# Kernel optimization log

Measured on AMD Instinct MI355X. Metric: run time of the kernel, lower is better.

The kernel has to match this reference:

```python
import jax, jax.numpy as jnp
import numpy as np

N = 100000      # nodes
E = 1000000     # edges (nnz of adj)
DIN = 128
DOUT = 64
MAX_W = 0.05    # max_weight in project_column_stochastic


def setup_inputs() -> dict:
    key = jax.random.key(0)
    k1, k2, k3, k4 = jax.random.split(key, 4)
    x = jax.random.normal(k1, (N, DIN), dtype=jnp.float32)
    edge_index = jax.random.randint(k2, (2, E), 0, N)  # [2, E] (row, col) of sparse adj
    edge_vals = jax.random.uniform(k3, (E,), dtype=jnp.float32)
    # column-stochastic init, mirroring reset_parameters():
    # uniform(0,1) -> clamp(min=threshold=0, max=0.05) -> column normalize
    w = jax.random.uniform(k4, (DIN, DOUT), dtype=jnp.float32)
    w = jnp.clip(w, 0.0, MAX_W)
    w = w / jnp.clip(w.sum(axis=0, keepdims=True), 1e-8, None)
    bias = jnp.zeros((DOUT,), dtype=jnp.float32)
    return {"input": x, "edge_index": edge_index, "edge_vals": edge_vals,
            "weight": w, "bias": bias}


def reference(input, edge_index, edge_vals, weight, bias):
    # support = input @ weight  (dense projection)
    support = input @ weight                          # [N, DOUT]
    # output = spmm(adj, support): gather source rows, scale by nnz value,
    # scatter-add into destination rows.
    rows, cols = edge_index[0], edge_index[1]
    msgs = edge_vals[:, None] * support[cols]         # [E, DOUT]
    out = jax.ops.segment_sum(msgs, rows, num_segments=input.shape[0])  # [N, DOUT]
    return out + bias
```

## Files before the change

kernel.cpp:

```cpp
#include <hip/hip_runtime.h>
#include <hip/hip_bf16.h>

#define DIN 128
#define DOUT 64
#define BROWS 256
#define MAXBKT 512
#define NGEMM 391
#define PART_BLOCK 512
#define PART_VPT 8
#define PART_CHUNK (PART_BLOCK * PART_VPT)
#define CAP 3584
#define ACC_VPT 4
#define WSTRIDE 136

typedef short short8 __attribute__((ext_vector_type(8)));
typedef float f32x4 __attribute__((ext_vector_type(4)));

union U4S8 { uint4 u; short8 s; };
union BF2U { __hip_bfloat162 h; unsigned int u; };

__device__ inline unsigned int f2bf(float f) {
    union { float f; unsigned int u; } v; v.f = f;
    unsigned int u = v.u;
    u += 0x7fffu + ((u >> 16) & 1u);
    return u >> 16;
}

struct PartSmem {
    int cnt[MAXBKT];
    int off[MAXBKT];
    int gbase[MAXBKT];
    int wsum[PART_BLOCK / 64];
    int lkey[PART_CHUNK];
    int lval[PART_CHUNK];
    short lbkt[PART_CHUNK];
};
struct GemmSmem {
    unsigned short wlds[DOUT * WSTRIDE];
};
union FusedSmem {
    PartSmem p;
    GemmSmem g;
};

__global__ __launch_bounds__(512) void gemm_part_kernel(const float* __restrict__ x,
                                                        const float* __restrict__ w,
                                                        unsigned short* __restrict__ support,
                                                        int ntiles,
                                                        const int* __restrict__ rows,
                                                        const int* __restrict__ cols,
                                                        const float* __restrict__ vals,
                                                        int* __restrict__ bucket_cursor,
                                                        uint2* __restrict__ tmp, int E) {
    __shared__ FusedSmem sm;
    int tid = threadIdx.x;
    if (blockIdx.x < NGEMM) {
        unsigned short* wlds = sm.g.wlds;
        for (int i = tid; i < DIN * DOUT; i += 512) {
            int k = i >> 6, n = i & 63;
            wlds[n * WSTRIDE + k] = (unsigned short)f2bf(w[i]);
        }
        __syncthreads();

        int lane = tid & 63, quad = lane >> 4, mlo = lane & 15;
        U4S8 wf[16];
#pragma unroll
        for (int kt = 0; kt < 4; ++kt)
#pragma unroll
            for (int nt = 0; nt < 4; ++nt)
                wf[kt * 4 + nt].u = *((const uint4*)(wlds + (nt * 16 + mlo) * WSTRIDE + kt * 32 + quad * 8));

        int wave0 = (blockIdx.x * 512 + tid) >> 6;
        int nwaves = NGEMM * 8;

        for (int tile = wave0; tile < ntiles; tile += nwaves) {
            const float4* p = (const float4*)(x + ((size_t)tile * 16 + mlo) * DIN + quad * 8);
            float4 fv[8];
#pragma unroll
            for (int kt = 0; kt < 4; ++kt) {
                fv[2 * kt]     = p[kt * 8];
                fv[2 * kt + 1] = p[kt * 8 + 1];
            }
            U4S8 af[4];
#pragma unroll
            for (int kt = 0; kt < 4; ++kt) {
                float4 a = fv[2 * kt], b = fv[2 * kt + 1];
                BF2U u0, u1, u2, u3;
                u0.h = __float22bfloat162_rn(make_float2(a.x, a.y));
                u1.h = __float22bfloat162_rn(make_float2(a.z, a.w));
                u2.h = __float22bfloat162_rn(make_float2(b.x, b.y));
                u3.h = __float22bfloat162_rn(make_float2(b.z, b.w));
                uint4 u; u.x = u0.u; u.y = u1.u; u.z = u2.u; u.w = u3.u;
                af[kt].u = u;
            }

            f32x4 acc[4] = {};
#pragma unroll
            for (int nt = 0; nt < 4; ++nt)
#pragma unroll
                for (int kt = 0; kt < 4; ++kt)
                    acc[nt] = __builtin_amdgcn_mfma_f32_16x16x32_bf16(af[kt].s, wf[kt * 4 + nt].s, acc[nt], 0, 0, 0);

#pragma unroll
            for (int nt = 0; nt < 4; ++nt)
#pragma unroll
                for (int r = 0; r < 4; ++r)
                    support[((size_t)tile * 16 + quad * 4 + r) * DOUT + nt * 16 + mlo] =
                        (unsigned short)f2bf(acc[nt][r]);
        }
    } else {
        int* cnt   = sm.p.cnt;
        int* off   = sm.p.off;
        int* gbase = sm.p.gbase;
        int* wsum  = sm.p.wsum;
        int* lkey  = sm.p.lkey;
        int* lval  = sm.p.lval;
        short* lbkt = sm.p.lbkt;

        int base = (blockIdx.x - NGEMM) * PART_CHUNK;

        cnt[tid] = 0;
        __syncthreads();

        int myr[PART_VPT], myc[PART_VPT], myrank[PART_VPT];
        float myv[PART_VPT];
#pragma unroll
        for (int i = 0; i < PART_VPT; ++i) {
            int e = base + i * PART_BLOCK + tid;
            if (e < E) {
                myr[i] = rows[e];
                myc[i] = cols[e];
                myv[i] = vals[e];
                myrank[i] = atomicAdd(&cnt[myr[i] >> 8], 1);
            }
        }
        __syncthreads();

        int c0 = cnt[tid];
        int lane = tid & 63, wid = tid >> 6;
        int ts = c0;
        for (int o = 1; o < 64; o <<= 1) {
            int t = __shfl_up(ts, o);
            if (lane >= o) ts += t;
        }
        if (lane == 63) wsum[wid] = ts;
        __syncthreads();
        int wb = 0;
        for (int w2 = 0; w2 < wid; ++w2) wb += wsum[w2];
        off[tid] = wb + ts - c0;
        if (c0 > 0) gbase[tid] = atomicAdd(&bucket_cursor[tid], c0);
        __syncthreads();

        int total = off[MAXBKT - 1] + cnt[MAXBKT - 1];

#pragma unroll
        for (int i = 0; i < PART_VPT; ++i) {
            int e = base + i * PART_BLOCK + tid;
            if (e < E) {
                int b = myr[i] >> 8;
                int pos = off[b] + myrank[i];
                lkey[pos] = ((myr[i] & (BROWS - 1)) << 17) | myc[i];
                lval[pos] = __float_as_int(myv[i]);
                lbkt[pos] = (short)b;
            }
        }
        __syncthreads();

        for (int s = tid; s < total; s += PART_BLOCK) {
            int b = lbkt[s];
            int pos = gbase[b] + (s - off[b]);
            if (pos < CAP)
                tmp[(size_t)b * CAP + pos] = make_uint2((unsigned)lkey[s], (unsigned)lval[s]);
        }
    }
}

__global__ __launch_bounds__(1024) void accum_kernel(const int* __restrict__ bucket_cursor,
                                                     const uint2* __restrict__ tmp,
                                                     const unsigned short* __restrict__ support,
                                                     const float* __restrict__ bias,
                                                     float* __restrict__ out, int N) {
    __shared__ int cnt[BROWS];
    __shared__ int rstart[BROWS];
    __shared__ int cur[BROWS];
    __shared__ int wsum4[4];
    __shared__ uint2 list[CAP];

    int b = blockIdx.x;
    int rbase = b * BROWS;
    int nrows = min(BROWS, N - rbase);
    int tid = threadIdx.x, lane = tid & 63, wv = tid >> 6;
    int start = b * CAP;
    int end = start + min(bucket_cursor[b], CAP);

    if (tid < BROWS) cnt[tid] = 0;
    __syncthreads();

    uint2 kv[ACC_VPT];
#pragma unroll
    for (int i = 0; i < ACC_VPT; ++i) {
        int s = start + i * 1024 + tid;
        if (s < end) {
            kv[i] = tmp[s];
            atomicAdd(&cnt[kv[i].x >> 17], 1);
        }
    }
    for (int s = start + ACC_VPT * 1024 + tid; s < end; s += 1024)
        atomicAdd(&cnt[tmp[s].x >> 17], 1);
    __syncthreads();

    int v = 0, incl = 0;
    if (tid < BROWS) {
        v = cnt[tid]; incl = v;
        for (int o = 1; o < 64; o <<= 1) {
            int t = __shfl_up(incl, o);
            if (lane >= o) incl += t;
        }
        if (lane == 63) wsum4[wv] = incl;
    }
    __syncthreads();
    if (tid < BROWS) {
        int wb = 0;
        for (int w = 0; w < wv; ++w) wb += wsum4[w];
        int st = wb + incl - v;
        rstart[tid] = st;
        cur[tid] = st;
    }
    __syncthreads();

#pragma unroll
    for (int i = 0; i < ACC_VPT; ++i) {
        int s = start + i * 1024 + tid;
        if (s < end) {
            int p = atomicAdd(&cur[kv[i].x >> 17], 1);
            if (p < CAP) list[p] = kv[i];
        }
    }
    for (int s = start + ACC_VPT * 1024 + tid; s < end; s += 1024) {
        uint2 k2 = tmp[s];
        int p = atomicAdd(&cur[k2.x >> 17], 1);
        if (p < CAP) list[p] = k2;
    }
    __syncthreads();

    int half = lane >> 5, cl = lane & 31;
    float2 bl = ((const float2*)bias)[cl];
    for (int rp = wv * 2 + half; rp < nrows; rp += 32) {
        int s = min(rstart[rp], CAP);
        int e2 = min(s + cnt[rp], CAP);
        float a0 = 0.f, a1 = 0.f, c0 = 0.f, c1 = 0.f;
        for (; s + 4 <= e2; s += 4) {
            uint2 ea = list[s], eb = list[s + 1], ec = list[s + 2], ed = list[s + 3];
            unsigned ga = *((const unsigned*)(support + (size_t)(ea.x & 0x1FFFF) * DOUT) + cl);
            unsigned gb = *((const unsigned*)(support + (size_t)(eb.x & 0x1FFFF) * DOUT) + cl);
            unsigned gc = *((const unsigned*)(support + (size_t)(ec.x & 0x1FFFF) * DOUT) + cl);
            unsigned gd = *((const unsigned*)(support + (size_t)(ed.x & 0x1FFFF) * DOUT) + cl);
            float va = __uint_as_float(ea.y), vb = __uint_as_float(eb.y);
            float vc = __uint_as_float(ec.y), vd = __uint_as_float(ed.y);
            a0 = fmaf(va, __uint_as_float(ga << 16), a0);
            a1 = fmaf(va, __uint_as_float(ga & 0xffff0000u), a1);
            c0 = fmaf(vb, __uint_as_float(gb << 16), c0);
            c1 = fmaf(vb, __uint_as_float(gb & 0xffff0000u), c1);
            a0 = fmaf(vc, __uint_as_float(gc << 16), a0);
            a1 = fmaf(vc, __uint_as_float(gc & 0xffff0000u), a1);
            c0 = fmaf(vd, __uint_as_float(gd << 16), c0);
            c1 = fmaf(vd, __uint_as_float(gd & 0xffff0000u), c1);
        }
        for (; s < e2; ++s) {
            uint2 ea = list[s];
            unsigned ga = *((const unsigned*)(support + (size_t)(ea.x & 0x1FFFF) * DOUT) + cl);
            float va = __uint_as_float(ea.y);
            a0 = fmaf(va, __uint_as_float(ga << 16), a0);
            a1 = fmaf(va, __uint_as_float(ga & 0xffff0000u), a1);
        }
        float2 o;
        o.x = a0 + c0 + bl.x;
        o.y = a1 + c1 + bl.y;
        *((float2*)(out + (size_t)(rbase + rp) * DOUT) + cl) = o;
    }
}

extern "C" void kernel_launch(void* const* d_in, const int* in_sizes, int n_in,
                              void* d_out, int out_size, void* d_ws, size_t ws_size,
                              hipStream_t stream) {
    const float* x    = (const float*)d_in[0];
    const int*   ei   = (const int*)d_in[1];
    const float* ev   = (const float*)d_in[2];
    const float* w    = (const float*)d_in[3];
    const float* bias = (const float*)d_in[4];
    float* out = (float*)d_out;

    const int N = in_sizes[0] / DIN;
    const int E = in_sizes[2];
    const int* rows = ei;
    const int* cols = ei + E;
    const int nbuckets = (N + BROWS - 1) / BROWS;

    char* ws = (char*)d_ws;
    size_t off = 0;
    auto take = [&](size_t bytes) { char* p = ws + off; off = (off + bytes + 255) & ~(size_t)255; return p; };
    unsigned short* support       = (unsigned short*)take((size_t)N * DOUT * sizeof(unsigned short));
    int*            bucket_cursor = (int*)take(MAXBKT * sizeof(int));
    uint2*          tmp           = (uint2*)take((size_t)nbuckets * CAP * sizeof(uint2));
    (void)ws_size;

    hipMemsetAsync(bucket_cursor, 0, MAXBKT * sizeof(int), stream);

    int ntiles = N / 16;
    int npart = (E + PART_CHUNK - 1) / PART_CHUNK;
    gemm_part_kernel<<<NGEMM + npart, 512, 0, stream>>>(x, w, support, ntiles,
                                                        rows, cols, ev,
                                                        bucket_cursor, tmp, E);

    accum_kernel<<<nbuckets, 1024, 0, stream>>>(bucket_cursor, tmp, support, bias, out, N);
}
```

Before: 140.7 us.

## Halve bucket size to 128 rows and use 512-thread accumulate blocks

Shrinks each destination bucket from 256 to 128 rows. That doubles the bucket count to 782 and cuts the per-bucket capacity to 2048, so the accumulate kernel can run with 512 threads and a smaller shared-memory list. The partition kernel now handles 1024 bucket counters, two per thread, in its scan. The aim is more, smaller accumulate blocks for better occupancy and load balance across CUs, plus a lower shared-memory footprint. The trade-offs are more global atomic cursor updates in the partition phase and a tighter overflow cap, since the leftover loop past ACC_VPT*512 entries was removed.

Result: no change. 143.4 us (+1.9%).

```diff
diff --git a/kernel.cpp b/kernel.cpp
--- a/kernel.cpp
+++ b/kernel.cpp
@@ -3,13 +3,14 @@
 
 #define DIN 128
 #define DOUT 64
-#define BROWS 256
-#define MAXBKT 512
+#define BROWS 128
+#define BSHIFT 7
+#define MAXBKT 1024
 #define NGEMM 391
 #define PART_BLOCK 512
 #define PART_VPT 8
 #define PART_CHUNK (PART_BLOCK * PART_VPT)
-#define CAP 3584
+#define CAP 2048
 #define ACC_VPT 4
 #define WSTRIDE 136
 
@@ -120,6 +121,7 @@
         int base = (blockIdx.x - NGEMM) * PART_CHUNK;
 
         cnt[tid] = 0;
+        cnt[tid + PART_BLOCK] = 0;
         __syncthreads();
 
         int myr[PART_VPT], myc[PART_VPT], myrank[PART_VPT];
@@ -131,14 +133,15 @@
                 myr[i] = rows[e];
                 myc[i] = cols[e];
                 myv[i] = vals[e];
-                myrank[i] = atomicAdd(&cnt[myr[i] >> 8], 1);
+                myrank[i] = atomicAdd(&cnt[myr[i] >> BSHIFT], 1);
             }
         }
         __syncthreads();
 
-        int c0 = cnt[tid];
+        int cA = cnt[2 * tid], cB = cnt[2 * tid + 1];
+        int pairc = cA + cB;
         int lane = tid & 63, wid = tid >> 6;
-        int ts = c0;
+        int ts = pairc;
         for (int o = 1; o < 64; o <<= 1) {
             int t = __shfl_up(ts, o);
             if (lane >= o) ts += t;
@@ -147,8 +150,11 @@
         __syncthreads();
         int wb = 0;
         for (int w2 = 0; w2 < wid; ++w2) wb += wsum[w2];
-        off[tid] = wb + ts - c0;
-        if (c0 > 0) gbase[tid] = atomicAdd(&bucket_cursor[tid], c0);
+        int ex = wb + ts - pairc;
+        off[2 * tid]     = ex;
+        off[2 * tid + 1] = ex + cA;
+        if (cA > 0) gbase[2 * tid]     = atomicAdd(&bucket_cursor[2 * tid], cA);
+        if (cB > 0) gbase[2 * tid + 1] = atomicAdd(&bucket_cursor[2 * tid + 1], cB);
         __syncthreads();
 
         int total = off[MAXBKT - 1] + cnt[MAXBKT - 1];
@@ -157,7 +163,7 @@
         for (int i = 0; i < PART_VPT; ++i) {
             int e = base + i * PART_BLOCK + tid;
             if (e < E) {
-                int b = myr[i] >> 8;
+                int b = myr[i] >> BSHIFT;
                 int pos = off[b] + myrank[i];
                 lkey[pos] = ((myr[i] & (BROWS - 1)) << 17) | myc[i];
                 lval[pos] = __float_as_int(myv[i]);
@@ -175,15 +181,15 @@
     }
 }
 
-__global__ __launch_bounds__(1024) void accum_kernel(const int* __restrict__ bucket_cursor,
-                                                     const uint2* __restrict__ tmp,
-                                                     const unsigned short* __restrict__ support,
-                                                     const float* __restrict__ bias,
-                                                     float* __restrict__ out, int N) {
+__global__ __launch_bounds__(512) void accum_kernel(const int* __restrict__ bucket_cursor,
+                                                    const uint2* __restrict__ tmp,
+                                                    const unsigned short* __restrict__ support,
+                                                    const float* __restrict__ bias,
+                                                    float* __restrict__ out, int N) {
     __shared__ int cnt[BROWS];
     __shared__ int rstart[BROWS];
     __shared__ int cur[BROWS];
-    __shared__ int wsum4[4];
+    __shared__ int wsum2[2];
     __shared__ uint2 list[CAP];
 
     int b = blockIdx.x;
@@ -199,14 +205,12 @@
     uint2 kv[ACC_VPT];
 #pragma unroll
     for (int i = 0; i < ACC_VPT; ++i) {
-        int s = start + i * 1024 + tid;
+        int s = start + i * 512 + tid;
         if (s < end) {
             kv[i] = tmp[s];
             atomicAdd(&cnt[kv[i].x >> 17], 1);
         }
     }
-    for (int s = start + ACC_VPT * 1024 + tid; s < end; s += 1024)
-        atomicAdd(&cnt[tmp[s].x >> 17], 1);
     __syncthreads();
 
     int v = 0, incl = 0;
@@ -216,12 +220,11 @@
             int t = __shfl_up(incl, o);
             if (lane >= o) incl += t;
         }
-        if (lane == 63) wsum4[wv] = incl;
+        if (lane == 63) wsum2[wv] = incl;
     }
     __syncthreads();
     if (tid < BROWS) {
-        int wb = 0;
-        for (int w = 0; w < wv; ++w) wb += wsum4[w];
+        int wb = (wv == 1) ? wsum2[0] : 0;
         int st = wb + incl - v;
         rstart[tid] = st;
         cur[tid] = st;
@@ -230,22 +233,17 @@
 
 #pragma unroll
     for (int i = 0; i < ACC_VPT; ++i) {
-        int s = start + i * 1024 + tid;
+        int s = start + i * 512 + tid;
         if (s < end) {
             int p = atomicAdd(&cur[kv[i].x >> 17], 1);
             if (p < CAP) list[p] = kv[i];
         }
     }
-    for (int s = start + ACC_VPT * 1024 + tid; s < end; s += 1024) {
-        uint2 k2 = tmp[s];
-        int p = atomicAdd(&cur[k2.x >> 17], 1);
-        if (p < CAP) list[p] = k2;
-    }
     __syncthreads();
 
     int half = lane >> 5, cl = lane & 31;
     float2 bl = ((const float2*)bias)[cl];
-    for (int rp = wv * 2 + half; rp < nrows; rp += 32) {
+    for (int rp = wv * 2 + half; rp < nrows; rp += 16) {
         int s = min(rstart[rp], CAP);
         int e2 = min(s + cnt[rp], CAP);
         float a0 = 0.f, a1 = 0.f, c0 = 0.f, c1 = 0.f;
@@ -312,5 +310,5 @@
                                                         rows, cols, ev,
                                                         bucket_cursor, tmp, E);
 
-    accum_kernel<<<nbuckets, 1024, 0, stream>>>(bucket_cursor, tmp, support, bias, out, N);
+    accum_kernel<<<nbuckets, 512, 0, stream>>>(bucket_cursor, tmp, support, bias, out, N);
 }
```

## Replace per-row sort in accumulate kernel with shared-memory atomic accumulation

Applied to the files above, without the earlier changes.

The accumulate kernel no longer counts, prefix-sums and scatters edges into a row-sorted shared list. Each wavefront now streams edges in their bucket order and atomically adds val*support into a 256x64 float accumulator held in shared memory, then writes rows out with the bias. This drops several barriers, the two passes over tmp and the shared-memory scatter. In exchange it issues one LDS atomic per edge per column, loads bf16 support as 2-byte scalars instead of paired 4-byte loads, and uses 64KB of LDS per block, which may cut occupancy.

Measured after the change: 545.0 us. 287% more time.

```diff
diff --git a/kernel.cpp b/kernel.cpp
--- a/kernel.cpp
+++ b/kernel.cpp
@@ -10,7 +10,6 @@
 #define PART_VPT 8
 #define PART_CHUNK (PART_BLOCK * PART_VPT)
 #define CAP 3584
-#define ACC_VPT 4
 #define WSTRIDE 136
 
 typedef short short8 __attribute__((ext_vector_type(8)));
@@ -180,11 +179,7 @@
                                                      const unsigned short* __restrict__ support,
                                                      const float* __restrict__ bias,
                                                      float* __restrict__ out, int N) {
-    __shared__ int cnt[BROWS];
-    __shared__ int rstart[BROWS];
-    __shared__ int cur[BROWS];
-    __shared__ int wsum4[4];
-    __shared__ uint2 list[CAP];
+    __shared__ float acc[BROWS * DOUT];
 
     int b = blockIdx.x;
     int rbase = b * BROWS;
@@ -193,91 +188,28 @@
     int start = b * CAP;
     int end = start + min(bucket_cursor[b], CAP);
 
-    if (tid < BROWS) cnt[tid] = 0;
+    for (int i = tid; i < BROWS * DOUT; i += 1024) acc[i] = 0.f;
     __syncthreads();
 
-    uint2 kv[ACC_VPT];
-#pragma unroll
-    for (int i = 0; i < ACC_VPT; ++i) {
-        int s = start + i * 1024 + tid;
-        if (s < end) {
-            kv[i] = tmp[s];
-            atomicAdd(&cnt[kv[i].x >> 17], 1);
-        }
-    }
-    for (int s = start + ACC_VPT * 1024 + tid; s < end; s += 1024)
-        atomicAdd(&cnt[tmp[s].x >> 17], 1);
-    __syncthreads();
-
-    int v = 0, incl = 0;
-    if (tid < BROWS) {
-        v = cnt[tid]; incl = v;
-        for (int o = 1; o < 64; o <<= 1) {
-            int t = __shfl_up(incl, o);
-            if (lane >= o) incl += t;
-        }
-        if (lane == 63) wsum4[wv] = incl;
+    float blv = bias[lane];
+
+    for (int s0 = start + wv * 64; s0 < end; s0 += 16 * 64) {
+        int nv = min(64, end - s0);
+#pragma unroll 4
+        for (int j = 0; j < nv; ++j) {
+            uint2 e = tmp[s0 + j];
+            int row = (int)(e.x >> 17);
+            int col = (int)(e.x & 0x1FFFF);
+            float val = __uint_as_float(e.y);
+            unsigned short sv = support[(size_t)col * DOUT + lane];
+            float su = __uint_as_float(((unsigned)sv) << 16);
+            atomicAdd(&acc[row * DOUT + lane], val * su);
+        }
     }
     __syncthreads();
-    if (tid < BROWS) {
-        int wb = 0;
-        for (int w = 0; w < wv; ++w) wb += wsum4[w];
-        int st = wb + incl - v;
-        rstart[tid] = st;
-        cur[tid] = st;
-    }
-    __syncthreads();
-
-#pragma unroll
-    for (int i = 0; i < ACC_VPT; ++i) {
-        int s = start + i * 1024 + tid;
-        if (s < end) {
-            int p = atomicAdd(&cur[kv[i].x >> 17], 1);
-            if (p < CAP) list[p] = kv[i];
-        }
-    }
-    for (int s = start + ACC_VPT * 1024 + tid; s < end; s += 1024) {
-        uint2 k2 = tmp[s];
-        int p = atomicAdd(&cur[k2.x >> 17], 1);
-        if (p < CAP) list[p] = k2;
-    }
-    __syncthreads();
-
-    int half = lane >> 5, cl = lane & 31;
-    float2 bl = ((const float2*)bias)[cl];
-    for (int rp = wv * 2 + half; rp < nrows; rp += 32) {
-        int s = min(rstart[rp], CAP);
-        int e2 = min(s + cnt[rp], CAP);
-        float a0 = 0.f, a1 = 0.f, c0 = 0.f, c1 = 0.f;
-        for (; s + 4 <= e2; s += 4) {
-            uint2 ea = list[s], eb = list[s + 1], ec = list[s + 2], ed = list[s + 3];
-            unsigned ga = *((const unsigned*)(support + (size_t)(ea.x & 0x1FFFF) * DOUT) + cl);
-            unsigned gb = *((const unsigned*)(support + (size_t)(eb.x & 0x1FFFF) * DOUT) + cl);
-            unsigned gc = *((const unsigned*)(support + (size_t)(ec.x & 0x1FFFF) * DOUT) + cl);
-            unsigned gd = *((const unsigned*)(support + (size_t)(ed.x & 0x1FFFF) * DOUT) + cl);
-            float va = __uint_as_float(ea.y), vb = __uint_as_float(eb.y);
-            float vc = __uint_as_float(ec.y), vd = __uint_as_float(ed.y);
-            a0 = fmaf(va, __uint_as_float(ga << 16), a0);
-            a1 = fmaf(va, __uint_as_float(ga & 0xffff0000u), a1);
-            c0 = fmaf(vb, __uint_as_float(gb << 16), c0);
-            c1 = fmaf(vb, __uint_as_float(gb & 0xffff0000u), c1);
-            a0 = fmaf(vc, __uint_as_float(gc << 16), a0);
-            a1 = fmaf(vc, __uint_as_float(gc & 0xffff0000u), a1);
-            c0 = fmaf(vd, __uint_as_float(gd << 16), c0);
-            c1 = fmaf(vd, __uint_as_float(gd & 0xffff0000u), c1);
-        }
-        for (; s < e2; ++s) {
-            uint2 ea = list[s];
-            unsigned ga = *((const unsigned*)(support + (size_t)(ea.x & 0x1FFFF) * DOUT) + cl);
-            float va = __uint_as_float(ea.y);
-            a0 = fmaf(va, __uint_as_float(ga << 16), a0);
-            a1 = fmaf(va, __uint_as_float(ga & 0xffff0000u), a1);
-        }
-        float2 o;
-        o.x = a0 + c0 + bl.x;
-        o.y = a1 + c1 + bl.y;
-        *((float2*)(out + (size_t)(rbase + rp) * DOUT) + cl) = o;
-    }
+
+    for (int r = wv; r < nrows; r += 16)
+        out[(size_t)(rbase + r) * DOUT + lane] = acc[r * DOUT + lane] + blv;
 }
 
 extern "C" void kernel_launch(void* const* d_in, const int* in_sizes, int n_in,
```
